# Kernel optimization log

Measured on AMD Instinct MI355X. Metric: run time of the kernel, lower is better.

Reference implementation:

```python
import jax, jax.numpy as jnp
import numpy as np

X_DIM = 20000   # number of input locations (x_l rows)
Y_DIM = 6000    # number of query locations (y_l rows)
REGION_DEG = 10.0  # lon/lat spread so every query has neighbors within 250 km
EARTH_DIAM = 2.0 * 6.378  # thousand-km diameter used by the source
THRESH = 0.25   # 250 km neighborhood threshold


def setup_inputs() -> dict:
    key = jax.random.key(0)
    k1, k2, k3 = jax.random.split(key, 3)
    x = jax.random.normal(k1, (X_DIM, 1), dtype=jnp.float32)
    x_l = jax.random.uniform(k2, (X_DIM, 2), dtype=jnp.float32) * REGION_DEG
    y_l = jax.random.uniform(k3, (Y_DIM, 2), dtype=jnp.float32) * REGION_DEG
    return {"x": x, "x_l": x_l, "y_l": y_l}


def reference(x, x_l, y_l):
    # Training branch of GPR.call, vectorized over the y_dim python loop.
    d2r = jnp.pi / 180.0
    lon_x, lat_x = x_l[:, 0], x_l[:, 1]   # (X,)
    lon_y, lat_y = y_l[:, 0], y_l[:, 1]   # (Y,)
    # haversine terms, shape (Y, X)
    hav = jnp.sin((lat_x[None, :] - lat_y[:, None]) * d2r) ** 2
    hav = hav + (jnp.cos(lat_x * d2r)[None, :] * jnp.cos(lat_y * d2r)[:, None]
                 * jnp.sin((lon_x[None, :] - lon_y[:, None]) * d2r) ** 2)
    d = EARTH_DIAM * jnp.arcsin(jnp.sqrt(hav))  # great-circle distance (thousand km)
    # threshold + gather/scatter in source == masked weights here
    w = jnp.where(d < THRESH, d, 0.0)
    s = jnp.sum(w, axis=1, keepdims=True)        # (Y, 1) per-row normalizer
    L = jnp.where(s > 0, w / jnp.maximum(s, 1e-12), 0.0)  # (Y, X) sparse-ish weights
    m = (L @ x)[:, 0]                            # (Y,) squeezed mean
    # V = 0.001 * I  (noise=None path); returned value is diag_part(V)
    v_diag = jnp.full((y_l.shape[0],), 0.001, dtype=x.dtype)
    return m, v_diag
```

## Files before the change

kernel.cpp:

```cpp
#include <hip/hip_runtime.h>
#include <math.h>


#define TPB    256
#define YPB    4
#define NSTRIP 40
#define NLON   40
#define NCELLS (NSTRIP * NLON)
#define C_CELL   0.25f
#define INV_CELL 4.0f
#define RLAT     1.1250f

__device__ __forceinline__ float sin_poly(float a) {
    float t = a * a;
    return a * fmaf(t, fmaf(t, 8.3333333e-3f, -0.16666667f), 1.0f);
}
__device__ __forceinline__ float cos_poly(float a) {
    float t = a * a;
    return fmaf(t, fmaf(t, fmaf(t, -1.3888889e-3f, 4.1666668e-2f), -0.5f), 1.0f);
}
__device__ __forceinline__ int cell_of(float lon, float lat) {
    int s = (int)(lat * INV_CELL); s = min(max(s, 0), NSTRIP - 1);
    int l = (int)(lon * INV_CELL); l = min(max(l, 0), NLON - 1);
    return s * NLON + l;
}


__global__ __launch_bounds__(TPB) void zero_kernel(int* __restrict__ histX,
                                                   int* __restrict__ histY) {
    for (int i = threadIdx.x; i < NCELLS; i += TPB) { histX[i] = 0; histY[i] = 0; }
}

__global__ __launch_bounds__(TPB) void hist_kernel(
    const float* __restrict__ x_l, const float* __restrict__ y_l,
    int* __restrict__ histX, int* __restrict__ histY, int nx, int ny)
{
    int i = blockIdx.x * TPB + threadIdx.x;
    if (i < nx) {
        atomicAdd(&histX[cell_of(x_l[2 * i], x_l[2 * i + 1])], 1);
    } else if (i < nx + ny) {
        int j = i - nx;
        atomicAdd(&histY[cell_of(y_l[2 * j], y_l[2 * j + 1])], 1);
    }
}

__global__ __launch_bounds__(TPB) void scan_kernel(
    const int* __restrict__ histX, const int* __restrict__ histY,
    int* __restrict__ csX, int* __restrict__ csY,
    int* __restrict__ curX, int* __restrict__ curY)
{
    const int CHUNK = (NCELLS + TPB - 1) / TPB;
    __shared__ int sums[TPB];
    const int* hist      = (blockIdx.x == 0) ? histX : histY;
    int*       cellStart = (blockIdx.x == 0) ? csX  : csY;
    int*       cursor    = (blockIdx.x == 0) ? curX : curY;

    int tid = threadIdx.x;
    int base = tid * CHUNK;
    int local[7];
    int s = 0;
    #pragma unroll
    for (int j = 0; j < CHUNK; ++j) {
        int idx = base + j;
        int v = (idx < NCELLS) ? hist[idx] : 0;
        local[j] = s; s += v;
    }
    sums[tid] = s;
    __syncthreads();
    for (int off = 1; off < TPB; off <<= 1) {
        int t = (tid >= off) ? sums[tid - off] : 0;
        __syncthreads();
        sums[tid] += t;
        __syncthreads();
    }
    int excl = (tid > 0) ? sums[tid - 1] : 0;
    #pragma unroll
    for (int j = 0; j < CHUNK; ++j) {
        int idx = base + j;
        if (idx < NCELLS) { cellStart[idx] = excl + local[j]; cursor[idx] = excl + local[j]; }
    }
    if (tid == TPB - 1) cellStart[NCELLS] = sums[TPB - 1];
}

__global__ __launch_bounds__(TPB) void scatter_kernel(
    const float* __restrict__ x, const float* __restrict__ x_l,
    const float* __restrict__ y_l,
    int* __restrict__ curX, int* __restrict__ curY,
    float4* __restrict__ sortedA, float2* __restrict__ sortedRaw,
    float*  __restrict__ sortedX,
    float2* __restrict__ sortedYL, int* __restrict__ sortedYIdx,
    int nx, int ny)
{
    const float d2r = 0.017453292519943295f;
    int i = blockIdx.x * TPB + threadIdx.x;
    if (i < nx) {
        float lon = x_l[2 * i], lat = x_l[2 * i + 1];
        int pos = atomicAdd(&curX[cell_of(lon, lat)], 1);
        float al = lat * d2r, ao = lon * d2r;
        sortedA[pos]   = make_float4(sin_poly(al), cos_poly(al),
                                     sin_poly(ao), cos_poly(ao));
        sortedRaw[pos] = make_float2(lon, lat);
        sortedX[pos]   = x[i];
    } else if (i < nx + ny) {
        int j = i - nx;
        float lon = y_l[2 * j], lat = y_l[2 * j + 1];
        int pos = atomicAdd(&curY[cell_of(lon, lat)], 1);
        sortedYL[pos]   = make_float2(lon, lat);
        sortedYIdx[pos] = j;
    }
}


__global__ __launch_bounds__(TPB) void gpr_binned(
    const float4* __restrict__ sortedA,
    const float2* __restrict__ sortedRaw,
    const float*  __restrict__ sortedX,
    const int*    __restrict__ cellStart,
    const float2* __restrict__ sortedYL,
    const int*    __restrict__ sortedYIdx,
    float* __restrict__ out, int ny, float Hcut, float HcutM)
{
    const int tid  = threadIdx.x;
    const int wave = tid >> 6;
    const int lane = tid & 63;
    const int j    = blockIdx.x * YPB + wave;

    const float d2r    = 0.017453292519943295f;
    const float r2d    = 57.29577951308232f;
    const float THRESH = 0.25f;
    const float DIAM   = 12.756f;
    const float DIAM6  = 12.756f / 6.0f;
    const float EPS_H  = 5e-8f;

    int   yidx  = 0;
    float lon_y = 0.0f, lat_y = 0.0f;
    if (j < ny) {
        yidx = sortedYIdx[j];
        float2 p = sortedYL[j];
        lon_y = p.x; lat_y = p.y;
    }
    const float sly   = sin_poly(lat_y * d2r);
    const float cly   = cos_poly(lat_y * d2r);
    const float slony = sin_poly(lon_y * d2r);
    const float clony = cos_poly(lon_y * d2r);

    float accw = 0.0f, accwx = 0.0f;

    const int s0 = max(0,          (int)floorf((lat_y - RLAT) * INV_CELL));
    const int s1 = min(NSTRIP - 1, (int)floorf((lat_y + RLAT) * INV_CELL));

    for (int s = s0; s <= s1; ++s) {
        float slo = s * C_CELL, shi = slo + C_CELL;
        float dmin = fmaxf(0.0f, fmaxf(slo - lat_y, lat_y - shi));
        float de   = fmaxf(0.0f, dmin - 3e-3f);
        float sd_  = sin_poly(de * d2r);
        float rem  = HcutM - sd_ * sd_;
        if (rem <= 0.0f) continue;
        float ccm = cos_poly(fminf(shi, 10.0f) * d2r) * cly * 0.999999f;
        float W   = asinf(fminf(1.0f, sqrtf(rem / ccm))) * r2d + 4e-3f;
        int lo = min(NLON - 1, max(0, (int)floorf((lon_y - W) * INV_CELL)));
        int hi = min(NLON - 1, max(0, (int)floorf((lon_y + W) * INV_CELL)));
        int p0 = cellStart[s * NLON + lo];
        int p1 = cellStart[s * NLON + hi + 1];

        for (int k = p0 + lane; k < p1; k += 64) {
            float4 e  = sortedA[k];
            float  xv = sortedX[k];

            float sl  = fmaf(e.x, cly,   -(e.y * sly));
            float sd  = fmaf(e.z, clony, -(e.w * slony));
            float cxy = e.y * cly;
            float hav = fmaf(sl, sl, cxy * (sd * sd));

            float tb  = hav - Hcut;
            float r   = __builtin_amdgcn_sqrtf(hav);
            float d   = r * fmaf(hav, DIAM6, DIAM);

            float w;
            if (__builtin_expect(fabsf(tb) < EPS_H, 0)) {
                float2 raw = sortedRaw[k];
                float lonx = raw.x, latx = raw.y;

                float dlat = __fsub_rn(latx, lat_y);
                float alat = __fmul_rn(dlat, d2r);
                float slf  = (float)sin((double)alat);
                float h1   = __fmul_rn(slf, slf);

                float axl  = __fmul_rn(latx,  d2r);
                float ayl  = __fmul_rn(lat_y, d2r);
                float cxf  = (float)cos((double)axl);
                float cyf  = (float)cos((double)ayl);
                float cc   = __fmul_rn(cxf, cyf);

                float dlon = __fsub_rn(lonx, lon_y);
                float alon = __fmul_rn(dlon, d2r);
                float sdf  = (float)sin((double)alon);
                float h2   = __fmul_rn(sdf, sdf);

                float hv   = __fadd_rn(h1, __fmul_rn(cc, h2));
                float r32  = (float)sqrt((double)hv);
                float as32 = (float)asin((double)r32);
                float dnp  = __fmul_rn(DIAM, as32);
                w = (dnp < THRESH) ? dnp : 0.0f;
            } else {
                w = (tb < 0.0f) ? d : 0.0f;
            }

            accw += w;
            accwx = fmaf(w, xv, accwx);
        }
    }

    #pragma unroll
    for (int off = 32; off > 0; off >>= 1) {
        accw  += __shfl_xor(accw,  off, 64);
        accwx += __shfl_xor(accwx, off, 64);
    }

    if (lane == 0 && j < ny) {
        float m = (accw > 0.0f) ? (accwx / fmaxf(accw, 1e-12f)) : 0.0f;
        out[yidx]      = m;
        out[ny + yidx] = 0.001f;
    }
}


__global__ __launch_bounds__(TPB) void gpr_full(
    const float* __restrict__ x, const float* __restrict__ x_l,
    const float* __restrict__ y_l, float* __restrict__ out,
    int nx, int ny, float Hcut)
{
    __shared__ float4 tA[1024];
    __shared__ float  tX[1024];

    const int tid  = threadIdx.x;
    const int wave = tid >> 6;
    const int lane = tid & 63;
    const int y    = blockIdx.x * YPB + wave;

    const float d2r    = 0.017453292519943295f;
    const float THRESH = 0.25f;
    const float DIAM   = 12.756f;
    const float DIAM6  = 12.756f / 6.0f;
    const float EPS_H  = 5e-8f;

    float lon_y = 0.0f, lat_y = 0.0f;
    if (y < ny) { lon_y = y_l[2 * y]; lat_y = y_l[2 * y + 1]; }
    const float sly   = sin_poly(lat_y * d2r);
    const float cly   = cos_poly(lat_y * d2r);
    const float slony = sin_poly(lon_y * d2r);
    const float clony = cos_poly(lon_y * d2r);

    float accw = 0.0f, accwx = 0.0f;

    const int ntiles = (nx + 1023) / 1024;
    for (int t = 0; t < ntiles; ++t) {
        const int base = t * 1024;
        __syncthreads();
        #pragma unroll
        for (int jj = 0; jj < 1024 / TPB; ++jj) {
            int idx = jj * TPB + tid, i = base + idx;
            if (i < nx) {
                float lon = x_l[2 * i], lat = x_l[2 * i + 1];
                tA[idx] = make_float4(sin_poly(lat * d2r), cos_poly(lat * d2r),
                                      sin_poly(lon * d2r), cos_poly(lon * d2r));
                tX[idx] = x[i];
            }
        }
        __syncthreads();

        const int tn = min(1024, nx - base);
        for (int k = lane; k < tn; k += 64) {
            float4 e  = tA[k];
            float  xv = tX[k];
            float sl  = fmaf(e.x, cly,   -(e.y * sly));
            float sd  = fmaf(e.z, clony, -(e.w * slony));
            float cxy = e.y * cly;
            float hav = fmaf(sl, sl, cxy * (sd * sd));
            float tb  = hav - Hcut;
            float r   = __builtin_amdgcn_sqrtf(hav);
            float d   = r * fmaf(hav, DIAM6, DIAM);
            float w;
            if (__builtin_expect(fabsf(tb) < EPS_H, 0)) {
                int   i    = base + k;
                float lonx = x_l[2 * i], latx = x_l[2 * i + 1];
                float dlat = __fsub_rn(latx, lat_y);
                float alat = __fmul_rn(dlat, d2r);
                float slf  = (float)sin((double)alat);
                float h1   = __fmul_rn(slf, slf);
                float axl  = __fmul_rn(latx,  d2r);
                float ayl  = __fmul_rn(lat_y, d2r);
                float cxf  = (float)cos((double)axl);
                float cyf  = (float)cos((double)ayl);
                float cc   = __fmul_rn(cxf, cyf);
                float dlon = __fsub_rn(lonx, lon_y);
                float alon = __fmul_rn(dlon, d2r);
                float sdf  = (float)sin((double)alon);
                float h2   = __fmul_rn(sdf, sdf);
                float hv   = __fadd_rn(h1, __fmul_rn(cc, h2));
                float r32  = (float)sqrt((double)hv);
                float as32 = (float)asin((double)r32);
                float dnp  = __fmul_rn(DIAM, as32);
                w = (dnp < THRESH) ? dnp : 0.0f;
            } else {
                w = (tb < 0.0f) ? d : 0.0f;
            }
            accw += w;
            accwx = fmaf(w, xv, accwx);
        }
    }

    #pragma unroll
    for (int off = 32; off > 0; off >>= 1) {
        accw  += __shfl_xor(accw,  off, 64);
        accwx += __shfl_xor(accwx, off, 64);
    }

    if (lane == 0 && y < ny) {
        float m = (accw > 0.0f) ? (accwx / fmaxf(accw, 1e-12f)) : 0.0f;
        out[y]      = m;
        out[ny + y] = 0.001f;
    }
}


extern "C" void kernel_launch(void* const* d_in, const int* in_sizes, int n_in,
                              void* d_out, int out_size, void* d_ws, size_t ws_size,
                              hipStream_t stream) {
    const float* x   = (const float*)d_in[0];
    const float* x_l = (const float*)d_in[1];
    const float* y_l = (const float*)d_in[2];
    float* out = (float*)d_out;

    const int nx = in_sizes[0];
    const int ny = in_sizes[2] / 2;

    double th = 0.25 / 12.756;
    double s  = sin(th);
    float Hcut  = (float)(s * s);
    float HcutM = (float)(s * s * 1.001);

    size_t offA   = 0;
    size_t offRaw = offA   + (size_t)nx * sizeof(float4);
    size_t offYL  = offRaw + (size_t)nx * sizeof(float2);
    size_t offX   = offYL  + (size_t)ny * sizeof(float2);
    size_t offYI  = offX   + (size_t)nx * sizeof(float);
    size_t offHX  = offYI  + (size_t)ny * sizeof(int);
    size_t offHY  = offHX  + (size_t)NCELLS * sizeof(int);
    size_t offCSX = offHY  + (size_t)NCELLS * sizeof(int);
    size_t offCSY = offCSX + (size_t)(NCELLS + 1) * sizeof(int);
    size_t offCuX = offCSY + (size_t)(NCELLS + 1) * sizeof(int);
    size_t offCuY = offCuX + (size_t)NCELLS * sizeof(int);
    size_t total  = offCuY + (size_t)NCELLS * sizeof(int);

    const int blocks = (ny + YPB - 1) / YPB;

    if (ws_size >= total) {
        float4* sortedA    = (float4*)((char*)d_ws + offA);
        float2* sortedRaw  = (float2*)((char*)d_ws + offRaw);
        float2* sortedYL   = (float2*)((char*)d_ws + offYL);
        float*  sortedX    = (float*) ((char*)d_ws + offX);
        int*    sortedYIdx = (int*)   ((char*)d_ws + offYI);
        int*    histX      = (int*)   ((char*)d_ws + offHX);
        int*    histY      = (int*)   ((char*)d_ws + offHY);
        int*    csX        = (int*)   ((char*)d_ws + offCSX);
        int*    csY        = (int*)   ((char*)d_ws + offCSY);
        int*    curX       = (int*)   ((char*)d_ws + offCuX);
        int*    curY       = (int*)   ((char*)d_ws + offCuY);

        int nb = (nx + ny + TPB - 1) / TPB;
        zero_kernel<<<1, TPB, 0, stream>>>(histX, histY);
        hist_kernel<<<nb, TPB, 0, stream>>>(x_l, y_l, histX, histY, nx, ny);
        scan_kernel<<<2, TPB, 0, stream>>>(histX, histY, csX, csY, curX, curY);
        scatter_kernel<<<nb, TPB, 0, stream>>>(x, x_l, y_l, curX, curY,
                                               sortedA, sortedRaw, sortedX,
                                               sortedYL, sortedYIdx, nx, ny);
        gpr_binned<<<blocks, TPB, 0, stream>>>(sortedA, sortedRaw, sortedX,
                                               csX, sortedYL, sortedYIdx,
                                               out, ny, Hcut, HcutM);
    } else {
        gpr_full<<<blocks, TPB, 0, stream>>>(x, x_l, y_l, out, nx, ny, Hcut);
    }
}
```

Measured before the change: 91.37 us.

## Process two sorted queries per wave and pack x value into point record

Each wavefront now handles two adjacent spatially-sorted query points and sweeps the union of their candidate cell ranges. Every loaded point record is reused for both queries, which halves the number of waves and the global loads per query. The x value is packed into the float4 in place of cos(lat), which is rebuilt with a sqrt, so the separate sortedX stream disappears. The column window now uses a cheap asin approximation, and the rare exact-precision path moves into a noinline helper to relieve register pressure. In exchange each wave may scan extra points that only one of its two queries needs, and the fallback kernel loses its shared-memory tiling.

```diff
diff --git a/kernel.cpp b/kernel.cpp
--- a/kernel.cpp
+++ b/kernel.cpp
@@ -3,7 +3,6 @@
 
 
 #define TPB    256
-#define YPB    4
 #define NSTRIP 40
 #define NLON   40
 #define NCELLS (NSTRIP * NLON)
@@ -23,6 +22,33 @@
     int s = (int)(lat * INV_CELL); s = min(max(s, 0), NSTRIP - 1);
     int l = (int)(lon * INV_CELL); l = min(max(l, 0), NLON - 1);
     return s * NLON + l;
+}
+
+__device__ __attribute__((noinline)) float band_w(float lonx, float latx,
+                                                  float lony, float laty)
+{
+    const float d2r = 0.017453292519943295f;
+    float dlat = __fsub_rn(latx, laty);
+    float alat = __fmul_rn(dlat, d2r);
+    float slf  = (float)sin((double)alat);
+    float h1   = __fmul_rn(slf, slf);
+
+    float axl  = __fmul_rn(latx, d2r);
+    float ayl  = __fmul_rn(laty, d2r);
+    float cxf  = (float)cos((double)axl);
+    float cyf  = (float)cos((double)ayl);
+    float cc   = __fmul_rn(cxf, cyf);
+
+    float dlon = __fsub_rn(lonx, lony);
+    float alon = __fmul_rn(dlon, d2r);
+    float sdf  = (float)sin((double)alon);
+    float h2   = __fmul_rn(sdf, sdf);
+
+    float hv   = __fadd_rn(h1, __fmul_rn(cc, h2));
+    float r32  = (float)sqrt((double)hv);
+    float as32 = (float)asin((double)r32);
+    float dnp  = __fmul_rn(12.756f, as32);
+    return (dnp < 0.25f) ? dnp : 0.0f;
 }
 
 
@@ -87,7 +113,6 @@
     const float* __restrict__ y_l,
     int* __restrict__ curX, int* __restrict__ curY,
     float4* __restrict__ sortedA, float2* __restrict__ sortedRaw,
-    float*  __restrict__ sortedX,
     float2* __restrict__ sortedYL, int* __restrict__ sortedYIdx,
     int nx, int ny)
 {
@@ -97,10 +122,9 @@
         float lon = x_l[2 * i], lat = x_l[2 * i + 1];
         int pos = atomicAdd(&curX[cell_of(lon, lat)], 1);
         float al = lat * d2r, ao = lon * d2r;
-        sortedA[pos]   = make_float4(sin_poly(al), cos_poly(al),
-                                     sin_poly(ao), cos_poly(ao));
+        sortedA[pos]   = make_float4(sin_poly(al), sin_poly(ao),
+                                     cos_poly(ao), x[i]);
         sortedRaw[pos] = make_float2(lon, lat);
-        sortedX[pos]   = x[i];
     } else if (i < nx + ny) {
         int j = i - nx;
         float lon = y_l[2 * j], lat = y_l[2 * j + 1];
@@ -114,7 +138,6 @@
 __global__ __launch_bounds__(TPB) void gpr_binned(
     const float4* __restrict__ sortedA,
     const float2* __restrict__ sortedRaw,
-    const float*  __restrict__ sortedX,
     const int*    __restrict__ cellStart,
     const float2* __restrict__ sortedYL,
     const int*    __restrict__ sortedYIdx,
@@ -123,104 +146,129 @@
     const int tid  = threadIdx.x;
     const int wave = tid >> 6;
     const int lane = tid & 63;
-    const int j    = blockIdx.x * YPB + wave;
+    const int wid  = blockIdx.x * (TPB / 64) + wave;
+    const int j0   = 2 * wid;
+    const int j1   = j0 + 1;
+    if (j0 >= ny) return;
+    const bool has1 = (j1 < ny);
 
     const float d2r    = 0.017453292519943295f;
     const float r2d    = 57.29577951308232f;
-    const float THRESH = 0.25f;
     const float DIAM   = 12.756f;
     const float DIAM6  = 12.756f / 6.0f;
     const float EPS_H  = 5e-8f;
 
-    int   yidx  = 0;
-    float lon_y = 0.0f, lat_y = 0.0f;
-    if (j < ny) {
-        yidx = sortedYIdx[j];
-        float2 p = sortedYL[j];
-        lon_y = p.x; lat_y = p.y;
-    }
-    const float sly   = sin_poly(lat_y * d2r);
-    const float cly   = cos_poly(lat_y * d2r);
-    const float slony = sin_poly(lon_y * d2r);
-    const float clony = cos_poly(lon_y * d2r);
-
-    float accw = 0.0f, accwx = 0.0f;
-
-    const int s0 = max(0,          (int)floorf((lat_y - RLAT) * INV_CELL));
-    const int s1 = min(NSTRIP - 1, (int)floorf((lat_y + RLAT) * INV_CELL));
+    const int    yi0 = sortedYIdx[j0];
+    const float2 q0  = sortedYL[j0];
+    const int    yi1 = has1 ? sortedYIdx[j1] : yi0;
+    const float2 q1  = has1 ? sortedYL[j1] : q0;
+
+    const float lon0 = q0.x, lat0 = q0.y;
+    const float lon1 = q1.x, lat1 = q1.y;
+
+    const float sly0 = sin_poly(lat0 * d2r), cly0 = cos_poly(lat0 * d2r);
+    const float slo0 = sin_poly(lon0 * d2r), clo0 = cos_poly(lon0 * d2r);
+    const float sly1 = sin_poly(lat1 * d2r), cly1 = cos_poly(lat1 * d2r);
+    const float slo1 = sin_poly(lon1 * d2r), clo1 = cos_poly(lon1 * d2r);
+
+    float accw0 = 0.0f, accx0 = 0.0f, accw1 = 0.0f, accx1 = 0.0f;
+
+    const float latmin = fminf(lat0, lat1), latmax = fmaxf(lat0, lat1);
+    const int s0 = max(0,          (int)floorf((latmin - RLAT) * INV_CELL));
+    const int s1 = min(NSTRIP - 1, (int)floorf((latmax + RLAT) * INV_CELL));
 
     for (int s = s0; s <= s1; ++s) {
-        float slo = s * C_CELL, shi = slo + C_CELL;
-        float dmin = fmaxf(0.0f, fmaxf(slo - lat_y, lat_y - shi));
-        float de   = fmaxf(0.0f, dmin - 3e-3f);
-        float sd_  = sin_poly(de * d2r);
-        float rem  = HcutM - sd_ * sd_;
-        if (rem <= 0.0f) continue;
-        float ccm = cos_poly(fminf(shi, 10.0f) * d2r) * cly * 0.999999f;
-        float W   = asinf(fminf(1.0f, sqrtf(rem / ccm))) * r2d + 4e-3f;
-        int lo = min(NLON - 1, max(0, (int)floorf((lon_y - W) * INV_CELL)));
-        int hi = min(NLON - 1, max(0, (int)floorf((lon_y + W) * INV_CELL)));
-        int p0 = cellStart[s * NLON + lo];
-        int p1 = cellStart[s * NLON + hi + 1];
+        const float slo = s * C_CELL, shi = slo + C_CELL;
+        const float ccs = cos_poly(fminf(shi, 10.0f) * d2r) * 0.999999f;
+
+        int lo = NLON, hi = -1;
+        {
+            float dmin = fmaxf(0.0f, fmaxf(slo - lat0, lat0 - shi));
+            float de   = fmaxf(0.0f, dmin - 3e-3f);
+            float sp   = sin_poly(de * d2r);
+            float rem  = HcutM - sp * sp;
+            if (rem > 0.0f) {
+                float rr = __builtin_amdgcn_sqrtf(rem / (ccs * cly0));
+                float W  = rr * fmaf(rr * rr, 0.16666667f, 1.0f) * r2d + 4e-3f;
+                lo = min(lo, min(NLON - 1, max(0, (int)floorf((lon0 - W) * INV_CELL))));
+                hi = max(hi, min(NLON - 1, max(0, (int)floorf((lon0 + W) * INV_CELL))));
+            }
+        }
+        {
+            float dmin = fmaxf(0.0f, fmaxf(slo - lat1, lat1 - shi));
+            float de   = fmaxf(0.0f, dmin - 3e-3f);
+            float sp   = sin_poly(de * d2r);
+            float rem  = HcutM - sp * sp;
+            if (rem > 0.0f) {
+                float rr = __builtin_amdgcn_sqrtf(rem / (ccs * cly1));
+                float W  = rr * fmaf(rr * rr, 0.16666667f, 1.0f) * r2d + 4e-3f;
+                lo = min(lo, min(NLON - 1, max(0, (int)floorf((lon1 - W) * INV_CELL))));
+                hi = max(hi, min(NLON - 1, max(0, (int)floorf((lon1 + W) * INV_CELL))));
+            }
+        }
+        if (hi < lo) continue;
+
+        const int p0 = cellStart[s * NLON + lo];
+        const int p1 = cellStart[s * NLON + hi + 1];
 
         for (int k = p0 + lane; k < p1; k += 64) {
-            float4 e  = sortedA[k];
-            float  xv = sortedX[k];
-
-            float sl  = fmaf(e.x, cly,   -(e.y * sly));
-            float sd  = fmaf(e.z, clony, -(e.w * slony));
-            float cxy = e.y * cly;
-            float hav = fmaf(sl, sl, cxy * (sd * sd));
-
-            float tb  = hav - Hcut;
-            float r   = __builtin_amdgcn_sqrtf(hav);
-            float d   = r * fmaf(hav, DIAM6, DIAM);
-
-            float w;
-            if (__builtin_expect(fabsf(tb) < EPS_H, 0)) {
-                float2 raw = sortedRaw[k];
-                float lonx = raw.x, latx = raw.y;
-
-                float dlat = __fsub_rn(latx, lat_y);
-                float alat = __fmul_rn(dlat, d2r);
-                float slf  = (float)sin((double)alat);
-                float h1   = __fmul_rn(slf, slf);
-
-                float axl  = __fmul_rn(latx,  d2r);
-                float ayl  = __fmul_rn(lat_y, d2r);
-                float cxf  = (float)cos((double)axl);
-                float cyf  = (float)cos((double)ayl);
-                float cc   = __fmul_rn(cxf, cyf);
-
-                float dlon = __fsub_rn(lonx, lon_y);
-                float alon = __fmul_rn(dlon, d2r);
-                float sdf  = (float)sin((double)alon);
-                float h2   = __fmul_rn(sdf, sdf);
-
-                float hv   = __fadd_rn(h1, __fmul_rn(cc, h2));
-                float r32  = (float)sqrt((double)hv);
-                float as32 = (float)asin((double)r32);
-                float dnp  = __fmul_rn(DIAM, as32);
-                w = (dnp < THRESH) ? dnp : 0.0f;
-            } else {
-                w = (tb < 0.0f) ? d : 0.0f;
+            float4 e = sortedA[k];
+            float cl = __builtin_amdgcn_sqrtf(fmaf(-e.x, e.x, 1.0f));
+
+            {
+                float sl  = fmaf(e.x, cly0, -(cl * sly0));
+                float sd  = fmaf(e.y, clo0, -(e.z * slo0));
+                float hav = fmaf(sl, sl, (cl * cly0) * (sd * sd));
+                float tb  = hav - Hcut;
+                float r   = __builtin_amdgcn_sqrtf(hav);
+                float d   = r * fmaf(hav, DIAM6, DIAM);
+                float w;
+                if (__builtin_expect(fabsf(tb) < EPS_H, 0)) {
+                    float2 raw = sortedRaw[k];
+                    w = band_w(raw.x, raw.y, lon0, lat0);
+                } else {
+                    w = (tb < 0.0f) ? d : 0.0f;
+                }
+                accw0 += w;
+                accx0  = fmaf(w, e.w, accx0);
             }
-
-            accw += w;
-            accwx = fmaf(w, xv, accwx);
+            {
+                float sl  = fmaf(e.x, cly1, -(cl * sly1));
+                float sd  = fmaf(e.y, clo1, -(e.z * slo1));
+                float hav = fmaf(sl, sl, (cl * cly1) * (sd * sd));
+                float tb  = hav - Hcut;
+                float r   = __builtin_amdgcn_sqrtf(hav);
+                float d   = r * fmaf(hav, DIAM6, DIAM);
+                float w;
+                if (__builtin_expect(fabsf(tb) < EPS_H, 0)) {
+                    float2 raw = sortedRaw[k];
+                    w = band_w(raw.x, raw.y, lon1, lat1);
+                } else {
+                    w = (tb < 0.0f) ? d : 0.0f;
+                }
+                accw1 += w;
+                accx1  = fmaf(w, e.w, accx1);
+            }
         }
     }
 
     #pragma unroll
     for (int off = 32; off > 0; off >>= 1) {
-        accw  += __shfl_xor(accw,  off, 64);
-        accwx += __shfl_xor(accwx, off, 64);
-    }
-
-    if (lane == 0 && j < ny) {
-        float m = (accw > 0.0f) ? (accwx / fmaxf(accw, 1e-12f)) : 0.0f;
-        out[yidx]      = m;
-        out[ny + yidx] = 0.001f;
+        accw0 += __shfl_xor(accw0, off, 64);
+        accx0 += __shfl_xor(accx0, off, 64);
+        accw1 += __shfl_xor(accw1, off, 64);
+        accx1 += __shfl_xor(accx1, off, 64);
+    }
+
+    if (lane == 0) {
+        float m0 = (accw0 > 0.0f) ? (accx0 / fmaxf(accw0, 1e-12f)) : 0.0f;
+        out[yi0]      = m0;
+        out[ny + yi0] = 0.001f;
+        if (has1) {
+            float m1 = (accw1 > 0.0f) ? (accx1 / fmaxf(accw1, 1e-12f)) : 0.0f;
+            out[yi1]      = m1;
+            out[ny + yi1] = 0.001f;
+        }
     }
 }
 
@@ -230,16 +278,12 @@
     const float* __restrict__ y_l, float* __restrict__ out,
     int nx, int ny, float Hcut)
 {
-    __shared__ float4 tA[1024];
-    __shared__ float  tX[1024];
-
     const int tid  = threadIdx.x;
     const int wave = tid >> 6;
     const int lane = tid & 63;
-    const int y    = blockIdx.x * YPB + wave;
+    const int y    = blockIdx.x * 4 + wave;
 
     const float d2r    = 0.017453292519943295f;
-    const float THRESH = 0.25f;
     const float DIAM   = 12.756f;
     const float DIAM6  = 12.756f / 6.0f;
     const float EPS_H  = 5e-8f;
@@ -253,61 +297,24 @@
 
     float accw = 0.0f, accwx = 0.0f;
 
-    const int ntiles = (nx + 1023) / 1024;
-    for (int t = 0; t < ntiles; ++t) {
-        const int base = t * 1024;
-        __syncthreads();
-        #pragma unroll
-        for (int jj = 0; jj < 1024 / TPB; ++jj) {
-            int idx = jj * TPB + tid, i = base + idx;
-            if (i < nx) {
-                float lon = x_l[2 * i], lat = x_l[2 * i + 1];
-                tA[idx] = make_float4(sin_poly(lat * d2r), cos_poly(lat * d2r),
-                                      sin_poly(lon * d2r), cos_poly(lon * d2r));
-                tX[idx] = x[i];
-            }
-        }
-        __syncthreads();
-
-        const int tn = min(1024, nx - base);
-        for (int k = lane; k < tn; k += 64) {
-            float4 e  = tA[k];
-            float  xv = tX[k];
-            float sl  = fmaf(e.x, cly,   -(e.y * sly));
-            float sd  = fmaf(e.z, clony, -(e.w * slony));
-            float cxy = e.y * cly;
-            float hav = fmaf(sl, sl, cxy * (sd * sd));
-            float tb  = hav - Hcut;
-            float r   = __builtin_amdgcn_sqrtf(hav);
-            float d   = r * fmaf(hav, DIAM6, DIAM);
-            float w;
-            if (__builtin_expect(fabsf(tb) < EPS_H, 0)) {
-                int   i    = base + k;
-                float lonx = x_l[2 * i], latx = x_l[2 * i + 1];
-                float dlat = __fsub_rn(latx, lat_y);
-                float alat = __fmul_rn(dlat, d2r);
-                float slf  = (float)sin((double)alat);
-                float h1   = __fmul_rn(slf, slf);
-                float axl  = __fmul_rn(latx,  d2r);
-                float ayl  = __fmul_rn(lat_y, d2r);
-                float cxf  = (float)cos((double)axl);
-                float cyf  = (float)cos((double)ayl);
-                float cc   = __fmul_rn(cxf, cyf);
-                float dlon = __fsub_rn(lonx, lon_y);
-                float alon = __fmul_rn(dlon, d2r);
-                float sdf  = (float)sin((double)alon);
-                float h2   = __fmul_rn(sdf, sdf);
-                float hv   = __fadd_rn(h1, __fmul_rn(cc, h2));
-                float r32  = (float)sqrt((double)hv);
-                float as32 = (float)asin((double)r32);
-                float dnp  = __fmul_rn(DIAM, as32);
-                w = (dnp < THRESH) ? dnp : 0.0f;
-            } else {
-                w = (tb < 0.0f) ? d : 0.0f;
-            }
-            accw += w;
-            accwx = fmaf(w, xv, accwx);
-        }
+    for (int k = lane; k < nx; k += 64) {
+        float lonx = x_l[2 * k], latx = x_l[2 * k + 1];
+        float xv   = x[k];
+        float sl   = fmaf(sin_poly(latx * d2r), cly, -(cos_poly(latx * d2r) * sly));
+        float sd   = fmaf(sin_poly(lonx * d2r), clony, -(cos_poly(lonx * d2r) * slony));
+        float cxy  = cos_poly(latx * d2r) * cly;
+        float hav  = fmaf(sl, sl, cxy * (sd * sd));
+        float tb   = hav - Hcut;
+        float r    = __builtin_amdgcn_sqrtf(hav);
+        float d    = r * fmaf(hav, DIAM6, DIAM);
+        float w;
+        if (__builtin_expect(fabsf(tb) < EPS_H, 0)) {
+            w = band_w(lonx, latx, lon_y, lat_y);
+        } else {
+            w = (tb < 0.0f) ? d : 0.0f;
+        }
+        accw += w;
+        accwx = fmaf(w, xv, accwx);
     }
 
     #pragma unroll
@@ -343,8 +350,7 @@
     size_t offA   = 0;
     size_t offRaw = offA   + (size_t)nx * sizeof(float4);
     size_t offYL  = offRaw + (size_t)nx * sizeof(float2);
-    size_t offX   = offYL  + (size_t)ny * sizeof(float2);
-    size_t offYI  = offX   + (size_t)nx * sizeof(float);
+    size_t offYI  = offYL  + (size_t)ny * sizeof(float2);
     size_t offHX  = offYI  + (size_t)ny * sizeof(int);
     size_t offHY  = offHX  + (size_t)NCELLS * sizeof(int);
     size_t offCSX = offHY  + (size_t)NCELLS * sizeof(int);
@@ -353,13 +359,10 @@
     size_t offCuY = offCuX + (size_t)NCELLS * sizeof(int);
     size_t total  = offCuY + (size_t)NCELLS * sizeof(int);
 
-    const int blocks = (ny + YPB - 1) / YPB;
-
     if (ws_size >= total) {
         float4* sortedA    = (float4*)((char*)d_ws + offA);
         float2* sortedRaw  = (float2*)((char*)d_ws + offRaw);
         float2* sortedYL   = (float2*)((char*)d_ws + offYL);
-        float*  sortedX    = (float*) ((char*)d_ws + offX);
         int*    sortedYIdx = (int*)   ((char*)d_ws + offYI);
         int*    histX      = (int*)   ((char*)d_ws + offHX);
         int*    histY      = (int*)   ((char*)d_ws + offHY);
@@ -373,12 +376,15 @@
         hist_kernel<<<nb, TPB, 0, stream>>>(x_l, y_l, histX, histY, nx, ny);
         scan_kernel<<<2, TPB, 0, stream>>>(histX, histY, csX, csY, curX, curY);
         scatter_kernel<<<nb, TPB, 0, stream>>>(x, x_l, y_l, curX, curY,
-                                               sortedA, sortedRaw, sortedX,
+                                               sortedA, sortedRaw,
                                                sortedYL, sortedYIdx, nx, ny);
-        gpr_binned<<<blocks, TPB, 0, stream>>>(sortedA, sortedRaw, sortedX,
-                                               csX, sortedYL, sortedYIdx,
+        int nwaves = (ny + 1) / 2;
+        int blocks = (nwaves + (TPB / 64) - 1) / (TPB / 64);
+        gpr_binned<<<blocks, TPB, 0, stream>>>(sortedA, sortedRaw, csX,
+                                               sortedYL, sortedYIdx,
                                                out, ny, Hcut, HcutM);
     } else {
+        int blocks = (ny + 3) / 4;
         gpr_full<<<blocks, TPB, 0, stream>>>(x, x_l, y_l, out, nx, ny, Hcut);
     }
 }
```

New measurement: 97.92 us. 1.07x slower.
